# Optimization experiments

Measured on AMD Instinct MI355X. Metric: run time of the kernel, lower is better.

Reference implementation:

```python
import jax, jax.numpy as jnp
import numpy as np

NEG_SLOPE = 0.2  # PyG GATConv leaky_relu slope


def _embed(feats, W1, b1, W2, b2, Wc, bc):
    # collapse_esm (two plain Linears, no activation) then linear_comb
    esm = feats[..., 24:] @ W1 + b1
    esm = esm @ W2 + b2
    x = jnp.concatenate([feats[..., :24], esm], axis=-1)
    return x @ Wc + bc


def _gat_conv(x, src, dst, n, W, a_src, a_dst, b, concat):
    # PyG GATConv: project, per-edge attention logits, softmax over incoming edges at dst,
    # weighted scatter-sum. Self loops already included in (src, dst).
    H, C = a_src.shape
    h = (x @ W).reshape(-1, H, C)                 # [N,H,C]
    s = (h * a_src).sum(-1)                       # [N,H]
    d = (h * a_dst).sum(-1)                       # [N,H]
    e = jax.nn.leaky_relu(s[src] + d[dst], NEG_SLOPE)  # [E,H]
    m = jax.ops.segment_max(e, dst, num_segments=n)
    e = jnp.exp(e - m[dst])
    z = jax.ops.segment_sum(e, dst, num_segments=n)
    alpha = e / z[dst]                            # [E,H]
    out = jax.ops.segment_sum(h[src] * alpha[:, :, None], dst, num_segments=n)  # [N,H,C]
    out = out.reshape(n, H * C) if concat else out.mean(axis=1)
    return out + b


def setup_inputs() -> dict:
    key = jax.random.key(0)
    ks = jax.random.split(key, 24)
    N, E, B, F = 100000, 3200000, 8, 50
    NF, M1, M2, M3, CH = 1304, 652, 326, 350, 32
    L, H, HID = 3, 8, 4
    f32 = jnp.float32
    inp = {
        "node_features": jax.random.normal(ks[0], (N, NF), f32),
        "edge_index": jax.random.randint(ks[1], (2, E), 0, N, dtype=jnp.int32),
        "edge_attr": jax.random.normal(ks[2], (E, 8), f32),
        "frag_emb": jax.random.normal(ks[3], (B, F, NF), f32),
        "W_esm1": jax.random.normal(ks[4], (NF - 24, M1), f32) / np.sqrt(NF - 24),
        "b_esm1": jnp.zeros((M1,), f32),
        "W_esm2": jax.random.normal(ks[5], (M1, M2), f32) / np.sqrt(M1),
        "b_esm2": jnp.zeros((M2,), f32),
        "W_comb": jax.random.normal(ks[6], (M3, CH), f32) / np.sqrt(M3),
        "b_comb": jnp.zeros((CH,), f32),
        "gat1_W": jax.random.normal(ks[7], (L, CH, H * HID), f32) / np.sqrt(CH),
        "gat1_asrc": jax.random.normal(ks[8], (L, H, HID), f32) * 0.1,
        "gat1_adst": jax.random.normal(ks[9], (L, H, HID), f32) * 0.1,
        "gat1_b": jnp.zeros((L, H * HID), f32),
        "gat2_W": jax.random.normal(ks[10], (L, H * HID, CH), f32) / np.sqrt(H * HID),
        "gat2_asrc": jax.random.normal(ks[11], (L, 1, CH), f32) * 0.1,
        "gat2_adst": jax.random.normal(ks[12], (L, 1, CH), f32) * 0.1,
        "gat2_b": jnp.zeros((L, CH), f32),
        "W_fin": jax.random.normal(ks[13], (CH, 1), f32) / np.sqrt(CH),
        "b_fin": jnp.zeros((1,), f32),
    }
    return inp


def reference(node_features, edge_index, edge_attr, frag_emb,
              W_esm1, b_esm1, W_esm2, b_esm2, W_comb, b_comb,
              gat1_W, gat1_asrc, gat1_adst, gat1_b,
              gat2_W, gat2_asrc, gat2_adst, gat2_b,
              W_fin, b_fin):
    N = node_features.shape[0]
    loop = jnp.arange(N, dtype=edge_index.dtype)
    src = jnp.concatenate([edge_index[0], loop])  # self loops (PyG default)
    dst = jnp.concatenate([edge_index[1], loop])

    x = _embed(node_features, W_esm1, b_esm1, W_esm2, b_esm2, W_comb, b_comb)  # [N,32]
    for i in range(gat1_W.shape[0]):
        x = _gat_conv(x, src, dst, N, gat1_W[i], gat1_asrc[i], gat1_adst[i], gat1_b[i], True)
        x = jax.nn.elu(x)
        x = _gat_conv(x, src, dst, N, gat2_W[i], gat2_asrc[i], gat2_adst[i], gat2_b[i], False)

    ys = _embed(frag_emb, W_esm1, b_esm1, W_esm2, b_esm2, W_comb, b_comb)  # [B,F,32]
    B, F, C = ys.shape
    xb = x.reshape(B, N // B, C)                      # equal-size graphs
    A = jax.nn.softmax(jnp.einsum('bnd,bfd->bnf', xb, ys), axis=-1)
    p = jnp.einsum('bnf,bfd->bnd', A, ys)             # [B,n,32]
    return jax.nn.sigmoid(p @ W_fin + b_fin).squeeze(-1)  # [B,n]
```

## Files before the change

kernel.cpp:

```cpp
#include <hip/hip_runtime.h>
#include <hip/hip_bf16.h>

#define NF 1304
#define M1 652
#define M2 326
#define CH 32
#define NHEAD1 8
#define HID1 4
#define NLAYER 3
#define FRAG 50
#define NBATCH 8
#define DPAD 32

static inline int ceil_div(int a, int b){ return (a + b - 1)/b; }

__device__ __forceinline__ unsigned short f2h(float f){
  _Float16 h = (_Float16)f;
  unsigned short u;
  __builtin_memcpy(&u, &h, 2);
  return u;
}
__device__ __forceinline__ float h2f(unsigned short u){
  _Float16 h;
  __builtin_memcpy(&h, &u, 2);
  return (float)h;
}

#define TM 64
#define TN 64
#define TKK 16
__global__ __launch_bounds__(256) void gemm_bias(
    const float* __restrict__ A, int lda,
    const float* __restrict__ B, int ldb,
    const float* __restrict__ bias,
    float* __restrict__ C, int ldc,
    int M, int N, int K, int acc)
{
  __shared__ float As[TKK][TM + 1];
  __shared__ float Bs[TKK][TN];
  int tid = threadIdx.x;
  int tx = tid & 15, ty = tid >> 4;
  int row0 = blockIdx.y * TM, col0 = blockIdx.x * TN;
  float c[4][4] = {};
  for (int k0 = 0; k0 < K; k0 += TKK) {
    #pragma unroll
    for (int p = 0; p < 4; ++p) {
      int r = (tid >> 4) + p * 16;
      int kk = tid & 15;
      int gr = row0 + r, gk = k0 + kk;
      float v = 0.f;
      if (gr < M && gk < K) v = A[(long long)gr * lda + gk];
      As[kk][r] = v;
    }
    #pragma unroll
    for (int p = 0; p < 4; ++p) {
      int kk = (tid >> 6) + p * 4;
      int cc = tid & 63;
      int gk = k0 + kk, gc = col0 + cc;
      float v = 0.f;
      if (gk < K && gc < N) v = B[(long long)gk * ldb + gc];
      Bs[kk][cc] = v;
    }
    __syncthreads();
    #pragma unroll
    for (int kk = 0; kk < TKK; ++kk) {
      float a[4], b[4];
      #pragma unroll
      for (int i = 0; i < 4; ++i) a[i] = As[kk][ty + 16 * i];
      #pragma unroll
      for (int j = 0; j < 4; ++j) b[j] = Bs[kk][tx + 16 * j];
      #pragma unroll
      for (int i = 0; i < 4; ++i)
        #pragma unroll
        for (int j = 0; j < 4; ++j)
          c[i][j] += a[i] * b[j];
    }
    __syncthreads();
  }
  #pragma unroll
  for (int i = 0; i < 4; ++i) {
    int gr = row0 + ty + 16 * i;
    if (gr >= M) continue;
    #pragma unroll
    for (int j = 0; j < 4; ++j) {
      int gc = col0 + tx + 16 * j;
      if (gc >= N) continue;
      float v = c[i][j];
      if (bias) v += bias[gc];
      if (acc) v += C[(long long)gr * ldc + gc];
      C[(long long)gr * ldc + gc] = v;
    }
  }
}

__global__ void fold_misc_kernel(const float* __restrict__ Wc, const float* __restrict__ T1,
                                 const float* __restrict__ b1, const float* __restrict__ b2,
                                 const float* __restrict__ bc,
                                 float* __restrict__ Wbig, float* __restrict__ bfold)
{
  int tid = threadIdx.x;
  for (int i = tid; i < 24 * CH; i += 256) Wbig[i] = Wc[i];
  if (tid < CH) {
    float v = bc[tid];
    for (int k = 0; k < M2; ++k) v += b2[k] * Wc[(24 + k) * CH + tid];
    for (int i = 0; i < M1; ++i) v += b1[i] * T1[i * CH + tid];
    bfold[tid] = v;
  }
}

#define EK 64
__device__ __forceinline__ void gemm_n32_body(
    const float* __restrict__ A, int M, int K,
    const float* __restrict__ W, const float* __restrict__ bias,
    float* __restrict__ C, int bid,
    float (*As)[65], float (*Ws)[32])
{
  int tid = threadIdx.x;
  int row0 = bid * 64;
  int tx = tid & 7, ty = tid >> 3;
  float c0[4] = {}, c1[4] = {};
  for (int k0 = 0; k0 < K; k0 += EK) {
    #pragma unroll
    for (int p = 0; p < 4; ++p) {
      int q = tid + p * 256;
      int r = q >> 4, c4 = (q & 15) * 4;
      int gr = row0 + r, gk = k0 + c4;
      float4 v = make_float4(0.f, 0.f, 0.f, 0.f);
      if (gr < M) {
        if (gk + 3 < K) v = *(const float4*)&A[(long long)gr * K + gk];
        else {
          float t[4] = {0.f, 0.f, 0.f, 0.f};
          for (int i = 0; i < 4; ++i) if (gk + i < K) t[i] = A[(long long)gr * K + gk + i];
          v = make_float4(t[0], t[1], t[2], t[3]);
        }
      }
      As[r][c4 + 0] = v.x; As[r][c4 + 1] = v.y; As[r][c4 + 2] = v.z; As[r][c4 + 3] = v.w;
    }
    #pragma unroll
    for (int p = 0; p < 2; ++p) {
      int q = tid + p * 256;
      int r = q >> 3, c4 = (q & 7) * 4;
      int gk = k0 + r;
      float4 v = make_float4(0.f, 0.f, 0.f, 0.f);
      if (gk < K) v = *(const float4*)&W[(long long)gk * 32 + c4];
      *(float4*)&Ws[r][c4] = v;
    }
    __syncthreads();
    #pragma unroll
    for (int kk = 0; kk < EK; ++kk) {
      float4 b = *(const float4*)&Ws[kk][tx * 4];
      float a0 = As[ty * 2][kk], a1 = As[ty * 2 + 1][kk];
      c0[0] += a0 * b.x; c0[1] += a0 * b.y; c0[2] += a0 * b.z; c0[3] += a0 * b.w;
      c1[0] += a1 * b.x; c1[1] += a1 * b.y; c1[2] += a1 * b.z; c1[3] += a1 * b.w;
    }
    __syncthreads();
  }
  float4 bb = *(const float4*)&bias[tx * 4];
  int gr0 = row0 + ty * 2;
  if (gr0 < M) {
    float4 v = make_float4(c0[0] + bb.x, c0[1] + bb.y, c0[2] + bb.z, c0[3] + bb.w);
    *(float4*)&C[(long long)gr0 * 32 + tx * 4] = v;
  }
  if (gr0 + 1 < M) {
    float4 v = make_float4(c1[0] + bb.x, c1[1] + bb.y, c1[2] + bb.z, c1[3] + bb.w);
    *(float4*)&C[(long long)(gr0 + 1) * 32 + tx * 4] = v;
  }
}

__global__ __launch_bounds__(256) void gemm_n32(
    const float* __restrict__ A, int M, int K,
    const float* __restrict__ W, const float* __restrict__ bias,
    float* __restrict__ C)
{
  __shared__ float As[64][65];
  __shared__ float Ws[EK][32];
  gemm_n32_body(A, M, K, W, bias, C, blockIdx.x, As, Ws);
}

__global__ __launch_bounds__(256) void gemm_n32_rank(
    const float* __restrict__ A, int M, int K,
    const float* __restrict__ W, const float* __restrict__ bias,
    float* __restrict__ C,
    const int* __restrict__ ei, int E, int chunk,
    int* __restrict__ degp, int* __restrict__ rank)
{
  __shared__ float As[64][65];
  __shared__ float Ws[EK][32];
  gemm_n32_body(A, M, K, W, bias, C, blockIdx.x, As, Ws);
  int e0 = blockIdx.x * chunk;
  int e1 = e0 + chunk; if (e1 > E) e1 = E;
  for (int e = e0 + threadIdx.x; e < e1; e += 256)
    rank[e] = atomicAdd(&degp[(long long)ei[E + e] * DPAD], 1);
}

__global__ void zero_deg_kernel(int* __restrict__ degp, long long n)
{
  long long i = (long long)blockIdx.x * 256 + threadIdx.x;
  if (i < n) degp[i] = 0;
}
__global__ void partial_kernel(const int* __restrict__ degp, int N, int* __restrict__ partial)
{
  __shared__ int sd[256];
  int i = blockIdx.x * 256 + threadIdx.x;
  sd[threadIdx.x] = (i < N) ? degp[(long long)i * DPAD] : 0;
  __syncthreads();
  for (int off = 128; off > 0; off >>= 1) {
    if (threadIdx.x < off) sd[threadIdx.x] += sd[threadIdx.x + off];
    __syncthreads();
  }
  if (threadIdx.x == 0) partial[blockIdx.x] = sd[0];
}
__global__ void scanp_kernel(int* __restrict__ partial, int NB)
{
  __shared__ int sd[512];
  int t = threadIdx.x;
  int v = (t < NB) ? partial[t] : 0;
  sd[t] = v;
  __syncthreads();
  for (int off = 1; off < 512; off <<= 1) {
    int u = (t >= off) ? sd[t - off] : 0;
    __syncthreads();
    sd[t] += u;
    __syncthreads();
  }
  if (t < NB) partial[t] = sd[t] - v;
}
__global__ void scan_final_kernel(const int* __restrict__ degp, int N,
                                  const int* __restrict__ partial,
                                  int* __restrict__ rowptr)
{
  __shared__ int sd[256];
  int i = blockIdx.x * 256 + threadIdx.x;
  int t = threadIdx.x;
  int v = (i < N) ? degp[(long long)i * DPAD] : 0;
  sd[t] = v;
  __syncthreads();
  for (int off = 1; off < 256; off <<= 1) {
    int u = (t >= off) ? sd[t - off] : 0;
    __syncthreads();
    sd[t] += u;
    __syncthreads();
  }
  if (i < N) {
    int excl = partial[blockIdx.x] + sd[t] - v;
    rowptr[i] = excl;
    if (i == N - 1) rowptr[N] = excl + v;
  }
}
__global__ void scatter_plain_kernel(const int* __restrict__ ei, int E,
                                     const int* __restrict__ rowptr,
                                     const int* __restrict__ rank,
                                     int* __restrict__ csr)
{
  int e = blockIdx.x * 256 + threadIdx.x;
  if (e >= E) return;
  int dn = ei[E + e];
  csr[rowptr[dn] + rank[e]] = ei[e];
}

template<int H, int C>
__global__ __launch_bounds__(256) void proj_sd_kernel(
    const float* __restrict__ x, const float* __restrict__ W,
    const float* __restrict__ adst,
    unsigned* __restrict__ hp, float* __restrict__ dv, int N)
{
  __shared__ float Ws[CH][CH];
  __shared__ float al[CH];
  int tid = threadIdx.x;
  for (int i = tid; i < CH * CH; i += 256) Ws[i >> 5][i & 31] = W[i];
  if (tid < CH) al[tid] = adst[tid];
  __syncthreads();
  int n = blockIdx.x * 256 + tid;
  if (n >= N) return;
  float xr[CH];
  #pragma unroll
  for (int j = 0; j < CH / 4; ++j) {
    float4 v = *(const float4*)&x[(long long)n * CH + j * 4];
    xr[j * 4] = v.x; xr[j * 4 + 1] = v.y; xr[j * 4 + 2] = v.z; xr[j * 4 + 3] = v.w;
  }
  float hr[CH] = {};
  #pragma unroll
  for (int c = 0; c < CH; ++c) {
    float xc = xr[c];
    #pragma unroll
    for (int j4 = 0; j4 < CH / 4; ++j4) {
      float4 w = *(const float4*)&Ws[c][j4 * 4];
      hr[j4 * 4] += xc * w.x; hr[j4 * 4 + 1] += xc * w.y;
      hr[j4 * 4 + 2] += xc * w.z; hr[j4 * 4 + 3] += xc * w.w;
    }
  }
  unsigned pk[16];
  #pragma unroll
  for (int j = 0; j < 16; ++j)
    pk[j] = (unsigned)f2h(hr[2 * j]) | ((unsigned)f2h(hr[2 * j + 1]) << 16);
  uint4* hq = (uint4*)&hp[(long long)n * 16];
  #pragma unroll
  for (int j = 0; j < 4; ++j)
    hq[j] = make_uint4(pk[4 * j], pk[4 * j + 1], pk[4 * j + 2], pk[4 * j + 3]);
  #pragma unroll
  for (int hh = 0; hh < H; ++hh) {
    float dd = 0.f;
    #pragma unroll
    for (int c = 0; c < C; ++c) dd += hr[hh * C + c] * al[hh * C + c];
    dv[(long long)n * H + hh] = dd;
  }
}

template<int H, int C>
__global__ __launch_bounds__(256) void gat_gather_kernel(
    const int* __restrict__ rowptr, const int* __restrict__ csr,
    const unsigned* __restrict__ hp, const float* __restrict__ asrc,
    const float* __restrict__ dv, const float* __restrict__ bias,
    float* __restrict__ xout, int N, int do_elu)
{
  int wid = threadIdx.x >> 6;
  int lane = threadIdx.x & 63;
  int n = blockIdx.x * 4 + wid;
  if (n >= N) return;
  int cpair = lane & 15;
  int slot = lane >> 4;
  int ch = cpair * 2;
  int hh = (C == HID1) ? (cpair >> 1) : 0;
  float a0 = asrc[ch], a1 = asrc[ch + 1];
  float dn = dv[(long long)n * H + hh];

  auto sred = [&](float p) {
    p += __shfl_xor(p, 1, 64);
    if (C == CH) {
      p += __shfl_xor(p, 2, 64);
      p += __shfl_xor(p, 4, 64);
      p += __shfl_xor(p, 8, 64);
    }
    return p;
  };

  float acc0 = 0.f, acc1 = 0.f, z = 0.f;
  {
    unsigned u = hp[(long long)n * 16 + cpair];
    float h0 = h2f((unsigned short)(u & 0xffff));
    float h1 = h2f((unsigned short)(u >> 16));
    float s = sred(h0 * a0 + h1 * a1);
    if (slot == 0) {
      float lg = s + dn;
      lg = lg > 0.f ? lg : 0.2f * lg;
      float w = expf(lg);
      z = w; acc0 = w * h0; acc1 = w * h1;
    }
  }
  int start = rowptr[n], end = rowptr[n + 1];
  for (int base = start; base < end; base += 64) {
    int m = end - base; if (m > 64) m = 64;
    int idx = (base + lane < end) ? csr[base + lane] : 0;
    int k = slot;
    for (; k + 12 < m; k += 16) {
      int si0 = __shfl(idx, k, 64);
      int si1 = __shfl(idx, k + 4, 64);
      int si2 = __shfl(idx, k + 8, 64);
      int si3 = __shfl(idx, k + 12, 64);
      unsigned u0 = hp[(long long)si0 * 16 + cpair];
      unsigned u1 = hp[(long long)si1 * 16 + cpair];
      unsigned u2 = hp[(long long)si2 * 16 + cpair];
      unsigned u3 = hp[(long long)si3 * 16 + cpair];
      float h00 = h2f((unsigned short)(u0 & 0xffff)), h01 = h2f((unsigned short)(u0 >> 16));
      float h10 = h2f((unsigned short)(u1 & 0xffff)), h11 = h2f((unsigned short)(u1 >> 16));
      float h20 = h2f((unsigned short)(u2 & 0xffff)), h21 = h2f((unsigned short)(u2 >> 16));
      float h30 = h2f((unsigned short)(u3 & 0xffff)), h31 = h2f((unsigned short)(u3 >> 16));
      float s0 = sred(h00 * a0 + h01 * a1);
      float s1 = sred(h10 * a0 + h11 * a1);
      float s2 = sred(h20 * a0 + h21 * a1);
      float s3 = sred(h30 * a0 + h31 * a1);
      float lg0 = s0 + dn; lg0 = lg0 > 0.f ? lg0 : 0.2f * lg0;
      float lg1 = s1 + dn; lg1 = lg1 > 0.f ? lg1 : 0.2f * lg1;
      float lg2 = s2 + dn; lg2 = lg2 > 0.f ? lg2 : 0.2f * lg2;
      float lg3 = s3 + dn; lg3 = lg3 > 0.f ? lg3 : 0.2f * lg3;
      float w0 = expf(lg0), w1 = expf(lg1), w2 = expf(lg2), w3 = expf(lg3);
      z += (w0 + w1) + (w2 + w3);
      acc0 += w0 * h00 + w1 * h10 + w2 * h20 + w3 * h30;
      acc1 += w0 * h01 + w1 * h11 + w2 * h21 + w3 * h31;
    }
    for (; k < m; k += 4) {
      int si0 = __shfl(idx, k, 64);
      unsigned u0 = hp[(long long)si0 * 16 + cpair];
      float h00 = h2f((unsigned short)(u0 & 0xffff)), h01 = h2f((unsigned short)(u0 >> 16));
      float s0 = sred(h00 * a0 + h01 * a1);
      float lg0 = s0 + dn; lg0 = lg0 > 0.f ? lg0 : 0.2f * lg0;
      float w0 = expf(lg0);
      z += w0;
      acc0 += w0 * h00;
      acc1 += w0 * h01;
    }
  }
  acc0 += __shfl_xor(acc0, 16, 64); acc0 += __shfl_xor(acc0, 32, 64);
  acc1 += __shfl_xor(acc1, 16, 64); acc1 += __shfl_xor(acc1, 32, 64);
  z    += __shfl_xor(z, 16, 64);    z    += __shfl_xor(z, 32, 64);
  if (slot == 0) {
    float v0 = acc0 / z + bias[ch];
    float v1 = acc1 / z + bias[ch + 1];
    if (do_elu) {
      v0 = v0 > 0.f ? v0 : (expf(v0) - 1.f);
      v1 = v1 > 0.f ? v1 : (expf(v1) - 1.f);
    }
    *(float2*)&xout[(long long)n * 32 + ch] = make_float2(v0, v1);
  }
}

__global__ __launch_bounds__(256) void pool_kernel(
    const float* __restrict__ x, const float* __restrict__ ys,
    const float* __restrict__ Wfin, const float* __restrict__ bfin,
    float* __restrict__ out, int NB)
{
  __shared__ float ysl[FRAG][CH];
  __shared__ float tl[FRAG];
  int b = blockIdx.y;
  int tid = threadIdx.x;
  for (int idx = tid; idx < FRAG * CH; idx += 256)
    ysl[idx >> 5][idx & 31] = ys[(long long)b * FRAG * CH + idx];
  __syncthreads();
  if (tid < FRAG) {
    float t = 0.f;
    #pragma unroll
    for (int dd = 0; dd < CH; ++dd) t += ysl[tid][dd] * Wfin[dd];
    tl[tid] = t;
  }
  __syncthreads();
  int n = blockIdx.x * 256 + tid;
  if (n >= NB) return;
  const float* xr = x + ((long long)b * NB + n) * CH;
  float xreg[CH];
  #pragma unroll
  for (int dd = 0; dd < CH; ++dd) xreg[dd] = xr[dd];
  float mx = -1e30f;
  for (int f = 0; f < FRAG; ++f) {
    float l = 0.f;
    #pragma unroll
    for (int dd = 0; dd < CH; ++dd) l += xreg[dd] * ysl[f][dd];
    mx = fmaxf(mx, l);
  }
  float se = 0.f, sw = 0.f;
  for (int f = 0; f < FRAG; ++f) {
    float l = 0.f;
    #pragma unroll
    for (int dd = 0; dd < CH; ++dd) l += xreg[dd] * ysl[f][dd];
    float e = expf(l - mx);
    se += e; sw += e * tl[f];
  }
  float logit = sw / se + bfin[0];
  out[(long long)b * NB + n] = 1.f / (1.f + expf(-logit));
}

extern "C" void kernel_launch(void* const* d_in, const int* in_sizes, int n_in,
                              void* d_out, int out_size, void* d_ws, size_t ws_size,
                              hipStream_t stream)
{
  const float* feats = (const float*)d_in[0];
  const int*   ei    = (const int*)d_in[1];
  const float* frag  = (const float*)d_in[3];
  const float* W1    = (const float*)d_in[4];
  const float* b1    = (const float*)d_in[5];
  const float* W2    = (const float*)d_in[6];
  const float* b2    = (const float*)d_in[7];
  const float* Wc    = (const float*)d_in[8];
  const float* bc    = (const float*)d_in[9];
  const float* g1W   = (const float*)d_in[10];
  const float* g1as  = (const float*)d_in[11];
  const float* g1ad  = (const float*)d_in[12];
  const float* g1b   = (const float*)d_in[13];
  const float* g2W   = (const float*)d_in[14];
  const float* g2as  = (const float*)d_in[15];
  const float* g2ad  = (const float*)d_in[16];
  const float* g2b   = (const float*)d_in[17];
  const float* Wfin  = (const float*)d_in[18];
  const float* bfin  = (const float*)d_in[19];

  const int N  = in_sizes[0] / NF;
  const int E  = in_sizes[1] / 2;
  const int BF = in_sizes[3] / NF;
  const int NB = N / NBATCH;

  char* ws = (char*)d_ws;
  size_t off = 0;
  auto walloc = [&](size_t bytes) -> void* {
    void* p = ws + off;
    off += (bytes + 255) & ~(size_t)255;
    return p;
  };
  float*    T1     = (float*)walloc((size_t)M1 * CH * 4);
  float*    Wbig   = (float*)walloc((size_t)NF * CH * 4);
  float*    bfold  = (float*)walloc((size_t)CH * 4);
  float*    x0     = (float*)walloc((size_t)N * CH * 4);
  float*    x1     = (float*)walloc((size_t)N * CH * 4);
  unsigned* hbuf   = (unsigned*)walloc((size_t)N * 16 * 4);
  float*    dbuf   = (float*)walloc((size_t)N * NHEAD1 * 4);
  float*    ysb    = (float*)walloc((size_t)BF * CH * 4);
  int*      degp   = (int*)walloc((size_t)N * DPAD * 4);
  int*      rowptr = (int*)walloc((size_t)(N + 1) * 4);
  int*      rank   = (int*)walloc((size_t)E * 4);
  int*      part   = (int*)walloc((size_t)512 * 4);
  int*      csr    = (int*)walloc((size_t)E * 4);
  (void)ws_size; (void)n_in; (void)out_size;

  {
    dim3 g1(1, ceil_div(M1, TM));
    gemm_bias<<<g1, 256, 0, stream>>>(W2, M2, Wc + 24 * CH, CH, nullptr, T1, CH,
                                      M1, CH, M2, 0);
    dim3 g2(1, ceil_div(NF - 24, TM));
    gemm_bias<<<g2, 256, 0, stream>>>(W1, M1, T1, CH, nullptr, Wbig + 24 * CH, CH,
                                      NF - 24, CH, M1, 0);
    fold_misc_kernel<<<1, 256, 0, stream>>>(Wc, T1, b1, b2, bc, Wbig, bfold);
  }

  {
    long long npad = (long long)N * DPAD;
    zero_deg_kernel<<<(int)((npad + 255) / 256), 256, 0, stream>>>(degp, npad);
    int nEmbed = ceil_div(N, 64);
    int chunk = ceil_div(E, nEmbed);
    gemm_n32_rank<<<nEmbed, 256, 0, stream>>>(feats, N, NF, Wbig, bfold, x0,
                                              ei, E, chunk, degp, rank);
    int nb = ceil_div(N, 256);
    partial_kernel<<<nb, 256, 0, stream>>>(degp, N, part);
    scanp_kernel<<<1, 512, 0, stream>>>(part, nb);
    scan_final_kernel<<<nb, 256, 0, stream>>>(degp, N, part, rowptr);
    scatter_plain_kernel<<<ceil_div(E, 256), 256, 0, stream>>>(ei, E, rowptr, rank, csr);
  }

  gemm_n32<<<ceil_div(BF, 64), 256, 0, stream>>>(frag, BF, NF, Wbig, bfold, ysb);

  auto conv = [&](const float* xin, float* xout, const float* W, const float* as_,
                  const float* ad_, const float* bias, int H, int do_elu) {
    if (H == NHEAD1) {
      proj_sd_kernel<NHEAD1, HID1><<<ceil_div(N, 256), 256, 0, stream>>>(
          xin, W, ad_, hbuf, dbuf, N);
      gat_gather_kernel<NHEAD1, HID1><<<ceil_div(N, 4), 256, 0, stream>>>(
          rowptr, csr, hbuf, as_, dbuf, bias, xout, N, do_elu);
    } else {
      proj_sd_kernel<1, CH><<<ceil_div(N, 256), 256, 0, stream>>>(
          xin, W, ad_, hbuf, dbuf, N);
      gat_gather_kernel<1, CH><<<ceil_div(N, 4), 256, 0, stream>>>(
          rowptr, csr, hbuf, as_, dbuf, bias, xout, N, do_elu);
    }
  };

  for (int l = 0; l < NLAYER; ++l) {
    conv(x0, x1, g1W + l * CH * CH, g1as + l * NHEAD1 * HID1, g1ad + l * NHEAD1 * HID1,
         g1b + l * CH, NHEAD1, 1);
    conv(x1, x0, g2W + l * CH * CH, g2as + l * CH, g2ad + l * CH,
         g2b + l * CH, 1, 0);
  }

  pool_kernel<<<dim3(ceil_div(NB, 256), NBATCH), 256, 0, stream>>>(
      x0, ysb, Wfin, bfin, (float*)d_out, NB);
}
```

Before: 1.320 ms.

## Register-prefetch next K tile in embed GEMM and halve row tile

The fused embedding GEMM plus degree-rank kernel now uses 32-row tiles instead of 64, which doubles the block count. It prefetches the next A and W K-slices into registers while the current tile is being computed, so global loads overlap with FMAs. The aim is to hide memory latency on the large 100000x1304 feature read, which dominates this kernel. In exchange, each thread does less work per W load, uses more registers, and the edge-rank chunk per block gets smaller.

```diff
diff --git a/kernel.cpp b/kernel.cpp
--- a/kernel.cpp
+++ b/kernel.cpp
@@ -109,14 +109,15 @@
 }
 
 #define EK 64
-__device__ __forceinline__ void gemm_n32_body(
+__global__ __launch_bounds__(256) void gemm_n32(
     const float* __restrict__ A, int M, int K,
     const float* __restrict__ W, const float* __restrict__ bias,
-    float* __restrict__ C, int bid,
-    float (*As)[65], float (*Ws)[32])
-{
+    float* __restrict__ C)
+{
+  __shared__ float As[64][65];
+  __shared__ float Ws[EK][32];
   int tid = threadIdx.x;
-  int row0 = bid * 64;
+  int row0 = blockIdx.x * 64;
   int tx = tid & 7, ty = tid >> 3;
   float c0[4] = {}, c1[4] = {};
   for (int k0 = 0; k0 < K; k0 += EK) {
@@ -167,16 +168,6 @@
   }
 }
 
-__global__ __launch_bounds__(256) void gemm_n32(
-    const float* __restrict__ A, int M, int K,
-    const float* __restrict__ W, const float* __restrict__ bias,
-    float* __restrict__ C)
-{
-  __shared__ float As[64][65];
-  __shared__ float Ws[EK][32];
-  gemm_n32_body(A, M, K, W, bias, C, blockIdx.x, As, Ws);
-}
-
 __global__ __launch_bounds__(256) void gemm_n32_rank(
     const float* __restrict__ A, int M, int K,
     const float* __restrict__ W, const float* __restrict__ bias,
@@ -184,9 +175,78 @@
     const int* __restrict__ ei, int E, int chunk,
     int* __restrict__ degp, int* __restrict__ rank)
 {
-  __shared__ float As[64][65];
+  __shared__ float As[32][65];
   __shared__ float Ws[EK][32];
-  gemm_n32_body(A, M, K, W, bias, C, blockIdx.x, As, Ws);
+  int tid = threadIdx.x;
+  int row0 = blockIdx.x * 32;
+  int tx = tid & 7, ty = tid >> 3;
+  float4 pa[2], pw[2];
+  auto loadA = [&](int k0, float4* dst) {
+    #pragma unroll
+    for (int p = 0; p < 2; ++p) {
+      int q = tid + p * 256;
+      int r = q >> 4, c4 = (q & 15) * 4;
+      int gr = row0 + r, gk = k0 + c4;
+      float4 v = make_float4(0.f, 0.f, 0.f, 0.f);
+      if (gr < M) {
+        if (gk + 3 < K) v = *(const float4*)&A[(long long)gr * K + gk];
+        else {
+          float t[4] = {0.f, 0.f, 0.f, 0.f};
+          for (int i = 0; i < 4; ++i) if (gk + i < K) t[i] = A[(long long)gr * K + gk + i];
+          v = make_float4(t[0], t[1], t[2], t[3]);
+        }
+      }
+      dst[p] = v;
+    }
+  };
+  auto loadW = [&](int k0, float4* dst) {
+    #pragma unroll
+    for (int p = 0; p < 2; ++p) {
+      int q = tid + p * 256;
+      int r = q >> 3, c4 = (q & 7) * 4;
+      int gk = k0 + r;
+      float4 v = make_float4(0.f, 0.f, 0.f, 0.f);
+      if (gk < K) v = *(const float4*)&W[(long long)gk * 32 + c4];
+      dst[p] = v;
+    }
+  };
+  auto store = [&](const float4* sa, const float4* sw) {
+    #pragma unroll
+    for (int p = 0; p < 2; ++p) {
+      int q = tid + p * 256;
+      int r = q >> 4, c4 = (q & 15) * 4;
+      As[r][c4 + 0] = sa[p].x; As[r][c4 + 1] = sa[p].y;
+      As[r][c4 + 2] = sa[p].z; As[r][c4 + 3] = sa[p].w;
+      int rw = q >> 3, cw = (q & 7) * 4;
+      *(float4*)&Ws[rw][cw] = sw[p];
+    }
+  };
+
+  float c0[4] = {};
+  loadA(0, pa); loadW(0, pw);
+  store(pa, pw);
+  __syncthreads();
+  for (int k0 = 0; k0 < K; k0 += EK) {
+    bool more = (k0 + EK < K);
+    if (more) { loadA(k0 + EK, pa); loadW(k0 + EK, pw); }
+    #pragma unroll
+    for (int kk = 0; kk < EK; ++kk) {
+      float4 b = *(const float4*)&Ws[kk][tx * 4];
+      float a = As[ty][kk];
+      c0[0] += a * b.x; c0[1] += a * b.y; c0[2] += a * b.z; c0[3] += a * b.w;
+    }
+    __syncthreads();
+    if (more) {
+      store(pa, pw);
+      __syncthreads();
+    }
+  }
+  int gr = row0 + ty;
+  if (gr < M) {
+    float4 bb = *(const float4*)&bias[tx * 4];
+    float4 v = make_float4(c0[0] + bb.x, c0[1] + bb.y, c0[2] + bb.z, c0[3] + bb.w);
+    *(float4*)&C[(long long)gr * 32 + tx * 4] = v;
+  }
   int e0 = blockIdx.x * chunk;
   int e1 = e0 + chunk; if (e1 > E) e1 = E;
   for (int e = e0 + threadIdx.x; e < e1; e += 256)
@@ -512,7 +572,7 @@
   {
     long long npad = (long long)N * DPAD;
     zero_deg_kernel<<<(int)((npad + 255) / 256), 256, 0, stream>>>(degp, npad);
-    int nEmbed = ceil_div(N, 64);
+    int nEmbed = ceil_div(N, 32);
     int chunk = ceil_div(E, nEmbed);
     gemm_n32_rank<<<nEmbed, 256, 0, stream>>>(feats, N, NF, Wbig, bfold, x0,
                                               ei, E, chunk, degp, rank);
```

Result: faster. 1.281 ms (median of 2 runs) (-2.9%).

## Split node embedding GEMM into K-split row-per-thread partials plus reduce; separate rank kernel

Applied to the files above, without the earlier changes.

Replaces the tiled 64-row embedding GEMM, which also did the edge-rank atomics, with a K-split kernel. Each block caches a 328x32 slice of the folded weight in LDS and each thread computes two full 32-wide output rows. A separate reduce kernel sums the four partials and adds the bias. The edge-rank atomics move into their own kernel. This trades extra partial-buffer traffic (4x N x 32 floats) and uncoalesced per-thread row loads for more parallelism and register-level reuse of the weight.

```diff
diff --git a/kernel.cpp b/kernel.cpp
--- a/kernel.cpp
+++ b/kernel.cpp
@@ -11,6 +11,7 @@
 #define FRAG 50
 #define NBATCH 8
 #define DPAD 32
+#define QK 328
 
 static inline int ceil_div(int a, int b){ return (a + b - 1)/b; }
 
@@ -109,14 +110,15 @@
 }
 
 #define EK 64
-__device__ __forceinline__ void gemm_n32_body(
+__global__ __launch_bounds__(256) void gemm_n32(
     const float* __restrict__ A, int M, int K,
     const float* __restrict__ W, const float* __restrict__ bias,
-    float* __restrict__ C, int bid,
-    float (*As)[65], float (*Ws)[32])
-{
+    float* __restrict__ C)
+{
+  __shared__ float As[64][65];
+  __shared__ float Ws[EK][32];
   int tid = threadIdx.x;
-  int row0 = bid * 64;
+  int row0 = blockIdx.x * 64;
   int tx = tid & 7, ty = tid >> 3;
   float c0[4] = {}, c1[4] = {};
   for (int k0 = 0; k0 < K; k0 += EK) {
@@ -167,36 +169,99 @@
   }
 }
 
-__global__ __launch_bounds__(256) void gemm_n32(
-    const float* __restrict__ A, int M, int K,
-    const float* __restrict__ W, const float* __restrict__ bias,
-    float* __restrict__ C)
-{
-  __shared__ float As[64][65];
-  __shared__ float Ws[EK][32];
-  gemm_n32_body(A, M, K, W, bias, C, blockIdx.x, As, Ws);
-}
-
-__global__ __launch_bounds__(256) void gemm_n32_rank(
-    const float* __restrict__ A, int M, int K,
-    const float* __restrict__ W, const float* __restrict__ bias,
-    float* __restrict__ C,
-    const int* __restrict__ ei, int E, int chunk,
-    int* __restrict__ degp, int* __restrict__ rank)
-{
-  __shared__ float As[64][65];
-  __shared__ float Ws[EK][32];
-  gemm_n32_body(A, M, K, W, bias, C, blockIdx.x, As, Ws);
-  int e0 = blockIdx.x * chunk;
-  int e1 = e0 + chunk; if (e1 > E) e1 = E;
-  for (int e = e0 + threadIdx.x; e < e1; e += 256)
-    rank[e] = atomicAdd(&degp[(long long)ei[E + e] * DPAD], 1);
+__global__ __launch_bounds__(256) void embed_part(
+    const float* __restrict__ A, int M,
+    const float* __restrict__ W,
+    float* __restrict__ part)
+{
+  __shared__ float Wl[QK][32];
+  int q = blockIdx.y;
+  int k0 = q * QK;
+  int kn = (q == 3) ? (NF - 3 * QK) : QK;
+  int tid = threadIdx.x;
+  {
+    const float4* src = (const float4*)(W + (long long)k0 * 32);
+    float4* dst = (float4*)&Wl[0][0];
+    int nf4 = kn * 8;
+    for (int i = tid; i < nf4; i += 256) dst[i] = src[i];
+  }
+  __syncthreads();
+
+  int r0 = blockIdx.x * 512 + tid;
+  int r1 = r0 + 256;
+  bool v0 = r0 < M, v1 = r1 < M;
+  const float* a0p = A + (long long)(v0 ? r0 : 0) * NF + k0;
+  const float* a1p = A + (long long)(v1 ? r1 : 0) * NF + k0;
+  float4 acc0[8], acc1[8];
+  #pragma unroll
+  for (int c = 0; c < 8; ++c) {
+    acc0[c] = make_float4(0.f, 0.f, 0.f, 0.f);
+    acc1[c] = make_float4(0.f, 0.f, 0.f, 0.f);
+  }
+  int nf4 = kn >> 2;
+  for (int f4 = 0; f4 < nf4; ++f4) {
+    float4 a0 = *(const float4*)(a0p + f4 * 4);
+    float4 a1 = *(const float4*)(a1p + f4 * 4);
+    #pragma unroll
+    for (int j = 0; j < 4; ++j) {
+      float aj0 = (&a0.x)[j];
+      float aj1 = (&a1.x)[j];
+      const float4* wr = (const float4*)&Wl[f4 * 4 + j][0];
+      #pragma unroll
+      for (int c = 0; c < 8; ++c) {
+        float4 w = wr[c];
+        acc0[c].x += aj0 * w.x; acc0[c].y += aj0 * w.y;
+        acc0[c].z += aj0 * w.z; acc0[c].w += aj0 * w.w;
+        acc1[c].x += aj1 * w.x; acc1[c].y += aj1 * w.y;
+        acc1[c].z += aj1 * w.z; acc1[c].w += aj1 * w.w;
+      }
+    }
+  }
+  float* p = part + (long long)q * M * 32;
+  if (v0) {
+    float4* o = (float4*)(p + (long long)r0 * 32);
+    #pragma unroll
+    for (int c = 0; c < 8; ++c) o[c] = acc0[c];
+  }
+  if (v1) {
+    float4* o = (float4*)(p + (long long)r1 * 32);
+    #pragma unroll
+    for (int c = 0; c < 8; ++c) o[c] = acc1[c];
+  }
+}
+
+__global__ __launch_bounds__(256) void embed_reduce(
+    const float* __restrict__ part, const float* __restrict__ bias,
+    float* __restrict__ C, int M)
+{
+  long long i = (long long)blockIdx.x * 256 + threadIdx.x;
+  long long tot = (long long)M * 8;
+  if (i >= tot) return;
+  long long stride = tot;
+  const float4* p = (const float4*)part;
+  float4 v = p[i];
+  float4 v1 = p[i + stride];
+  float4 v2 = p[i + 2 * stride];
+  float4 v3 = p[i + 3 * stride];
+  float4 bb = ((const float4*)bias)[i & 7];
+  float4 o;
+  o.x = ((v.x + v1.x) + v2.x) + v3.x + bb.x;
+  o.y = ((v.y + v1.y) + v2.y) + v3.y + bb.y;
+  o.z = ((v.z + v1.z) + v2.z) + v3.z + bb.z;
+  o.w = ((v.w + v1.w) + v2.w) + v3.w + bb.w;
+  ((float4*)C)[i] = o;
 }
 
 __global__ void zero_deg_kernel(int* __restrict__ degp, long long n)
 {
   long long i = (long long)blockIdx.x * 256 + threadIdx.x;
   if (i < n) degp[i] = 0;
+}
+__global__ void rank_kernel(const int* __restrict__ ei, int E,
+                            int* __restrict__ degp, int* __restrict__ rank)
+{
+  int e = blockIdx.x * 256 + threadIdx.x;
+  if (e < E) rank[e] = atomicAdd(&degp[(long long)ei[E + e] * DPAD], 1);
 }
 __global__ void partial_kernel(const int* __restrict__ degp, int N, int* __restrict__ partial)
 {
@@ -497,6 +562,7 @@
   int*      rank   = (int*)walloc((size_t)E * 4);
   int*      part   = (int*)walloc((size_t)512 * 4);
   int*      csr    = (int*)walloc((size_t)E * 4);
+  float*    pembed = (float*)walloc((size_t)4 * N * CH * 4);
   (void)ws_size; (void)n_in; (void)out_size;
 
   {
@@ -510,13 +576,17 @@
   }
 
   {
+    dim3 g(ceil_div(N, 512), 4);
+    embed_part<<<g, 256, 0, stream>>>(feats, N, Wbig, pembed);
+    long long tot = (long long)N * 8;
+    embed_reduce<<<(int)((tot + 255) / 256), 256, 0, stream>>>(pembed, bfold, x0, N);
+  }
+
+  {
     long long npad = (long long)N * DPAD;
+    int nb = ceil_div(N, 256);
     zero_deg_kernel<<<(int)((npad + 255) / 256), 256, 0, stream>>>(degp, npad);
-    int nEmbed = ceil_div(N, 64);
-    int chunk = ceil_div(E, nEmbed);
-    gemm_n32_rank<<<nEmbed, 256, 0, stream>>>(feats, N, NF, Wbig, bfold, x0,
-                                              ei, E, chunk, degp, rank);
-    int nb = ceil_div(N, 256);
+    rank_kernel<<<ceil_div(E, 256), 256, 0, stream>>>(ei, E, degp, rank);
     partial_kernel<<<nb, 256, 0, stream>>>(degp, N, part);
     scanp_kernel<<<1, 512, 0, stream>>>(part, nb);
     scan_final_kernel<<<nb, 256, 0, stream>>>(degp, N, part, rowptr);
```

Measured after the change: 1.530 ms. 1.16x slower.
